# Optimization experiments

Measured on AMD Instinct MI355X. Metric: run time of the kernel, lower is better.

The kernel has to match this reference:

```python
import jax, jax.numpy as jnp
import numpy as np


def _gcn_conv(X, src, dst, norm, W, n_nodes):
    # gather + normalized aggregate (SpMM) then dense linear (GEMM)
    msg = X[src] * norm[:, None]                       # [E, F]
    agg = jax.ops.segment_sum(msg, dst, num_segments=n_nodes)  # [N, F]
    return agg @ W                                     # [N, F_out]


def setup_inputs() -> dict:
    key = jax.random.key(0)
    k1, k2, k3, k4, k5 = jax.random.split(key, 5)
    N, E, D_IN, D_HID, D_OUT = 50000, 800000, 128, 128, 64
    X = jax.random.normal(k1, (N, D_IN), dtype=jnp.float32)
    edge_index = jax.random.randint(k2, (2, E), 0, N, dtype=jnp.int64)
    s = 1.0 / np.sqrt(D_IN)
    W1 = jax.random.normal(k3, (D_IN, D_HID), dtype=jnp.float32) * s
    W2 = jax.random.normal(k4, (D_HID, D_HID), dtype=jnp.float32) * s
    W3 = jax.random.normal(k5, (D_HID, D_OUT), dtype=jnp.float32) * s
    return {"X": X, "edge_index": edge_index, "W1": W1, "W2": W2, "W3": W3}


def reference(X, edge_index, W1, W2, W3):
    n_nodes = X.shape[0]
    src, dst = edge_index[0], edge_index[1]
    # symmetric degree normalization D^-1/2 A D^-1/2 (degrees from edge list)
    ones = jnp.ones(src.shape[0], dtype=X.dtype)
    deg = jax.ops.segment_sum(ones, dst, num_segments=n_nodes)
    deg = jnp.maximum(deg, 1.0)
    dinv = jax.lax.rsqrt(deg)
    norm = dinv[src] * dinv[dst]                       # [E]
    h = jax.nn.relu(_gcn_conv(X, src, dst, norm, W1, n_nodes))
    h = jax.nn.relu(_gcn_conv(h, src, dst, norm, W2, n_nodes))
    h = jax.nn.relu(_gcn_conv(h, src, dst, norm, W3, n_nodes))
    return jax.nn.softmax(h, axis=-1)
```

## Files before the change

kernel.cpp:

```cpp
#include <hip/hip_runtime.h>
#include <hip/hip_bf16.h>

typedef __attribute__((ext_vector_type(8))) short short8;
typedef __attribute__((ext_vector_type(4))) short short4v;
typedef __attribute__((ext_vector_type(4))) float f32x4;

static inline size_t ws_align(size_t x) { return (x + 511) & ~((size_t)511); }

static __device__ inline unsigned short f2bf(float f) {
    __hip_bfloat16 h = __float2bfloat16(f);
    return __builtin_bit_cast(unsigned short, h);
}

__global__ void sniff_kernel(const unsigned short* __restrict__ w1,
                             const unsigned int* __restrict__ ei,
                             int* __restrict__ flags) {
    int i = threadIdx.x;
    unsigned e = (w1[2 * i] >> 7) & 0xFF;
    unsigned long long m1 = __ballot(e >= 100 && e <= 130);
    unsigned long long m2 = __ballot(ei[2 * i + 1] == 0u);
    if (i == 0) {
        flags[0] = (__popcll(m1) < 48) ? 1 : 0;
        flags[1] = (__popcll(m2) >= 48) ? 1 : 0;
    }
}

__global__ void hist_kernel(const int* __restrict__ ei, const int* __restrict__ flags,
                            int* __restrict__ counts, int* __restrict__ loff, int E) {
    int e = blockIdx.x * blockDim.x + threadIdx.x;
    if (e < E) {
        int d = flags[1] ? ei[2 * (size_t)E + 2 * e] : ei[(size_t)E + e];
        loff[e] = atomicAdd(&counts[d], 1);
    }
}

__global__ __launch_bounds__(256) void alloc_kernel(const int* __restrict__ counts,
                                                    float* __restrict__ dinv,
                                                    int* __restrict__ rowptr,
                                                    int* __restrict__ total, int N) {
    int n = blockIdx.x * blockDim.x + threadIdx.x;
    int lane = threadIdx.x & 63;
    int c = (n < N) ? counts[n] : 0;
    if (n < N) {
        int d = (c < 1) ? 1 : c;
        dinv[n] = rsqrtf((float)d);
    }
    int incl = c;
#pragma unroll
    for (int off = 1; off < 64; off <<= 1) {
        int v = __shfl_up(incl, off, 64);
        if (lane >= off) incl += v;
    }
    int wavetot = __shfl(incl, 63, 64);
    int base = 0;
    if (lane == 0) base = atomicAdd(total, wavetot);
    base = __shfl(base, 0, 64);
    if (n < N) rowptr[n] = base + incl - c;
}

__global__ void fill_kernel(const int* __restrict__ ei, const int* __restrict__ flags,
                            const float* __restrict__ dinv, const int* __restrict__ rowptr,
                            const int* __restrict__ loff, int2* __restrict__ edgedat, int E) {
    int e = blockIdx.x * blockDim.x + threadIdx.x;
    if (e < E) {
        int s, d;
        if (flags[1]) {
            s = ei[2 * e];
            d = ei[2 * (size_t)E + 2 * e];
        } else {
            s = ei[e];
            d = ei[(size_t)E + e];
        }
        int pos = rowptr[d] + loff[e];
        float wt = dinv[s] * dinv[d];
        edgedat[pos] = make_int2(s, __float_as_int(wt));
    }
}


template <int FOUT>
__global__ __launch_bounds__(256) void gemm_kernel(const void* __restrict__ Araw, int a_follows,
                                                   const void* __restrict__ Wraw,
                                                   const int* __restrict__ flags,
                                                   unsigned short* __restrict__ out, int Nrows) {
    constexpr int K = 128;
    constexpr int NT = FOUT / 16;
    constexpr int LDB = K + 8;
    __shared__ __align__(16) unsigned short bt[FOUT * LDB];

    const int tid = threadIdx.x;
    const int in_fp32 = flags[0];
    const int a_fp32 = a_follows & in_fp32;

    constexpr int TOT4 = K * FOUT / 4;
    if (in_fp32) {
        const float* Wf = (const float*)Wraw;
        for (int i = tid; i < TOT4; i += 256) {
            int idx = i * 4;
            int k = idx / FOUT;
            int n = idx & (FOUT - 1);
            float4 v = *(const float4*)(const void*)(Wf + idx);
            bt[(n + 0) * LDB + k] = f2bf(v.x);
            bt[(n + 1) * LDB + k] = f2bf(v.y);
            bt[(n + 2) * LDB + k] = f2bf(v.z);
            bt[(n + 3) * LDB + k] = f2bf(v.w);
        }
    } else {
        const unsigned short* Ws = (const unsigned short*)Wraw;
        for (int i = tid; i < TOT4; i += 256) {
            int idx = i * 4;
            int k = idx / FOUT;
            int n = idx & (FOUT - 1);
            short4v v = *(const short4v*)(const void*)(Ws + idx);
#pragma unroll
            for (int j = 0; j < 4; j++) bt[(n + j) * LDB + k] = ((const unsigned short*)&v)[j];
        }
    }

    const int wave = tid >> 6;
    const int lane = tid & 63;
    const int quad = lane >> 4;
    const int r16 = lane & 15;

    short8 afrag[2][4];
#pragma unroll
    for (int t = 0; t < 2; t++) {
        int arow = blockIdx.x * 128 + t * 64 + wave * 16 + r16;
        if (arow > Nrows - 1) arow = Nrows - 1;
        if (a_fp32) {
            const float* Ap = (const float*)Araw + (size_t)arow * K + quad * 8;
#pragma unroll
            for (int kk = 0; kk < 4; kk++) {
                float4 f0 = *(const float4*)(const void*)(Ap + kk * 32);
                float4 f1 = *(const float4*)(const void*)(Ap + kk * 32 + 4);
                short8 r;
                r[0] = (short)f2bf(f0.x); r[1] = (short)f2bf(f0.y);
                r[2] = (short)f2bf(f0.z); r[3] = (short)f2bf(f0.w);
                r[4] = (short)f2bf(f1.x); r[5] = (short)f2bf(f1.y);
                r[6] = (short)f2bf(f1.z); r[7] = (short)f2bf(f1.w);
                afrag[t][kk] = r;
            }
        } else {
            const unsigned short* Ap = (const unsigned short*)Araw + (size_t)arow * K + quad * 8;
#pragma unroll
            for (int kk = 0; kk < 4; kk++) afrag[t][kk] = *(const short8*)(const void*)(Ap + kk * 32);
        }
    }

    __syncthreads();

    f32x4 acc[2][NT];
#pragma unroll
    for (int t = 0; t < 2; t++)
#pragma unroll
        for (int nt = 0; nt < NT; nt++) acc[t][nt] = (f32x4){0.f, 0.f, 0.f, 0.f};

#pragma unroll
    for (int kk = 0; kk < 4; kk++) {
#pragma unroll
        for (int nt = 0; nt < NT; nt++) {
            short8 b = *(const short8*)(const void*)(&bt[(nt * 16 + r16) * LDB + kk * 32 + quad * 8]);
#pragma unroll
            for (int t = 0; t < 2; t++)
                acc[t][nt] = __builtin_amdgcn_mfma_f32_16x16x32_bf16(afrag[t][kk], b, acc[t][nt], 0, 0, 0);
        }
    }

#pragma unroll
    for (int t = 0; t < 2; t++) {
#pragma unroll
        for (int nt = 0; nt < NT; nt++) {
#pragma unroll
            for (int r = 0; r < 4; r++) {
                float v = acc[t][nt][r];
                float o = __shfl_xor(v, 1, 64);
                int row = blockIdx.x * 128 + t * 64 + wave * 16 + quad * 4 + r;
                if (((lane & 1) == 0) && row < Nrows) {
                    __hip_bfloat162 pk;
                    pk.x = __float2bfloat16(v);
                    pk.y = __float2bfloat16(o);
                    *(__hip_bfloat162*)(out + (size_t)row * FOUT + nt * 16 + r16) = pk;
                }
            }
        }
    }
}


__global__ __launch_bounds__(256) void spmm128_kernel(const int2* __restrict__ edgedat,
                                                      const int* __restrict__ rowptr,
                                                      const int* __restrict__ counts,
                                                      const __hip_bfloat162* __restrict__ Hin,
                                                      __hip_bfloat162* __restrict__ Hout, int N) {
    int wid = (blockIdx.x * 256 + threadIdx.x) >> 6;
    if (wid >= N) return;
    int lane = threadIdx.x & 63;
    int n = __builtin_amdgcn_readfirstlane(wid);
    int start = __builtin_amdgcn_readfirstlane(rowptr[n]);
    int len = __builtin_amdgcn_readfirstlane(counts[n]);
    float ax = 0.f, ay = 0.f;
    int j = 0;
    for (; j + 8 <= len; j += 8) {
        int2 ed[8];
        __hip_bfloat162 hv[8];
#pragma unroll
        for (int u = 0; u < 8; u++) ed[u] = edgedat[start + j + u];
#pragma unroll
        for (int u = 0; u < 8; u++) hv[u] = Hin[(size_t)ed[u].x * 64 + lane];
#pragma unroll
        for (int u = 0; u < 8; u++) {
            float w = __int_as_float(ed[u].y);
            ax += w * __bfloat162float(hv[u].x);
            ay += w * __bfloat162float(hv[u].y);
        }
    }
    for (; j + 4 <= len; j += 4) {
        int2 ed[4];
        __hip_bfloat162 hv[4];
#pragma unroll
        for (int u = 0; u < 4; u++) ed[u] = edgedat[start + j + u];
#pragma unroll
        for (int u = 0; u < 4; u++) hv[u] = Hin[(size_t)ed[u].x * 64 + lane];
#pragma unroll
        for (int u = 0; u < 4; u++) {
            float w = __int_as_float(ed[u].y);
            ax += w * __bfloat162float(hv[u].x);
            ay += w * __bfloat162float(hv[u].y);
        }
    }
    for (; j < len; j++) {
        int2 ed = edgedat[start + j];
        float wt = __int_as_float(ed.y);
        __hip_bfloat162 hv = Hin[(size_t)ed.x * 64 + lane];
        ax += wt * __bfloat162float(hv.x);
        ay += wt * __bfloat162float(hv.y);
    }
    __hip_bfloat162 pk;
    pk.x = __float2bfloat16(fmaxf(ax, 0.f));
    pk.y = __float2bfloat16(fmaxf(ay, 0.f));
    Hout[(size_t)n * 64 + lane] = pk;
}

__global__ __launch_bounds__(256) void spmm64_softmax_kernel(const int2* __restrict__ edgedat,
                                                             const int* __restrict__ rowptr,
                                                             const int* __restrict__ counts,
                                                             const __hip_bfloat16* __restrict__ Hin,
                                                             const int* __restrict__ flags,
                                                             void* __restrict__ Out, int N) {
    int wid = (blockIdx.x * 256 + threadIdx.x) >> 6;
    if (wid >= N) return;
    int lane = threadIdx.x & 63;
    int n = __builtin_amdgcn_readfirstlane(wid);
    int start = __builtin_amdgcn_readfirstlane(rowptr[n]);
    int len = __builtin_amdgcn_readfirstlane(counts[n]);
    float a = 0.f;
    int j = 0;
    for (; j + 8 <= len; j += 8) {
        int2 ed[8];
        float hv[8];
#pragma unroll
        for (int u = 0; u < 8; u++) ed[u] = edgedat[start + j + u];
#pragma unroll
        for (int u = 0; u < 8; u++) hv[u] = __bfloat162float(Hin[(size_t)ed[u].x * 64 + lane]);
#pragma unroll
        for (int u = 0; u < 8; u++) a += __int_as_float(ed[u].y) * hv[u];
    }
    for (; j + 4 <= len; j += 4) {
        int2 ed[4];
        float hv[4];
#pragma unroll
        for (int u = 0; u < 4; u++) ed[u] = edgedat[start + j + u];
#pragma unroll
        for (int u = 0; u < 4; u++) hv[u] = __bfloat162float(Hin[(size_t)ed[u].x * 64 + lane]);
#pragma unroll
        for (int u = 0; u < 4; u++) a += __int_as_float(ed[u].y) * hv[u];
    }
    for (; j < len; j++) {
        int2 ed = edgedat[start + j];
        a += __int_as_float(ed.y) * __bfloat162float(Hin[(size_t)ed.x * 64 + lane]);
    }
    a = fmaxf(a, 0.f);
    float m = a;
#pragma unroll
    for (int off = 32; off > 0; off >>= 1) m = fmaxf(m, __shfl_xor(m, off, 64));
    float e = __expf(a - m);
    float s = e;
#pragma unroll
    for (int off = 32; off > 0; off >>= 1) s += __shfl_xor(s, off, 64);
    float r = e / s;
    if (flags[0]) {
        ((float*)Out)[(size_t)n * 64 + lane] = r;
    } else {
        ((unsigned short*)Out)[(size_t)n * 64 + lane] = f2bf(r);
    }
}


extern "C" void kernel_launch(void* const* d_in, const int* in_sizes, int n_in,
                              void* d_out, int out_size, void* d_ws, size_t ws_size,
                              hipStream_t stream) {
    const void* X  = d_in[0];
    const int*  ei = (const int*)d_in[1];
    const void* W1 = d_in[2];
    const void* W2 = d_in[3];
    const void* W3 = d_in[4];

    const int N = in_sizes[0] / 128;
    const int E = in_sizes[1] / 2;

    char* ws = (char*)d_ws;
    size_t off = 0;
    int* counts = (int*)(ws + off);   off += ws_align((size_t)N * 4);
    int* total  = (int*)(ws + off);   off += ws_align(64);
    const size_t zero_bytes = off;
    int* flags    = (int*)(ws + off);   off += ws_align(64);
    int* rowptr   = (int*)(ws + off);   off += ws_align((size_t)N * 4);
    float* dinv   = (float*)(ws + off); off += ws_align((size_t)N * 4);
    int* loff     = (int*)(ws + off);   off += ws_align((size_t)E * 4);
    int2* edgedat = (int2*)(ws + off);  off += ws_align((size_t)E * 8);
    unsigned short* HA = (unsigned short*)(ws + off); off += ws_align((size_t)N * 128 * 2);
    unsigned short* HB = (unsigned short*)(ws + off); off += ws_align((size_t)N * 128 * 2);

    hipMemsetAsync(d_ws, 0, zero_bytes, stream);

    sniff_kernel<<<1, 64, 0, stream>>>((const unsigned short*)W1, (const unsigned int*)ei, flags);
    hist_kernel<<<(E + 255) / 256, 256, 0, stream>>>(ei, flags, counts, loff, E);
    alloc_kernel<<<(N + 255) / 256, 256, 0, stream>>>(counts, dinv, rowptr, total, N);
    fill_kernel<<<(E + 255) / 256, 256, 0, stream>>>(ei, flags, dinv, rowptr, loff, edgedat, E);

    const int gblocks = (N + 127) / 128;
    const int sblocks = (N * 64 + 255) / 256;

    gemm_kernel<128><<<gblocks, 256, 0, stream>>>(X, 1, W1, flags, HA, N);
    spmm128_kernel<<<sblocks, 256, 0, stream>>>(edgedat, rowptr, counts,
                                                (const __hip_bfloat162*)HA, (__hip_bfloat162*)HB, N);
    gemm_kernel<128><<<gblocks, 256, 0, stream>>>(HB, 0, W2, flags, HA, N);
    spmm128_kernel<<<sblocks, 256, 0, stream>>>(edgedat, rowptr, counts,
                                                (const __hip_bfloat162*)HA, (__hip_bfloat162*)HB, N);
    gemm_kernel<64><<<gblocks, 256, 0, stream>>>(HB, 0, W3, flags, HA, N);
    spmm64_softmax_kernel<<<sblocks, 256, 0, stream>>>(edgedat, rowptr, counts,
                                                       (const __hip_bfloat16*)HA, flags, d_out, N);
}
```

Before: 271.3 us.

## Split wave into edge groups with 16-byte row loads in SpMM kernels

Each SpMM wavefront now splits into lane groups (4 groups of 16 lanes for 128 features, 8 groups of 8 lanes for 64 features). Each lane loads 8 bf16 values with one 16-byte vector load, so several edges are gathered in parallel. Partial sums are combined with cross-group shuffles before writing, and the softmax is reduced over 8 lanes with vectorized output stores. This raises memory-level parallelism and cuts per-edge instruction count, at the cost of extra shuffle reductions and more registers.

```diff
diff --git a/kernel.cpp b/kernel.cpp
--- a/kernel.cpp
+++ b/kernel.cpp
@@ -10,6 +10,11 @@
 static __device__ inline unsigned short f2bf(float f) {
     __hip_bfloat16 h = __float2bfloat16(f);
     return __builtin_bit_cast(unsigned short, h);
+}
+
+static __device__ inline float bf2f(unsigned short u) {
+    unsigned int x = ((unsigned int)u) << 16;
+    return __builtin_bit_cast(float, x);
 }
 
 __global__ void sniff_kernel(const unsigned short* __restrict__ w1,
@@ -190,108 +195,156 @@
 __global__ __launch_bounds__(256) void spmm128_kernel(const int2* __restrict__ edgedat,
                                                       const int* __restrict__ rowptr,
                                                       const int* __restrict__ counts,
-                                                      const __hip_bfloat162* __restrict__ Hin,
-                                                      __hip_bfloat162* __restrict__ Hout, int N) {
+                                                      const unsigned short* __restrict__ Hin,
+                                                      unsigned short* __restrict__ Hout, int N) {
     int wid = (blockIdx.x * 256 + threadIdx.x) >> 6;
     if (wid >= N) return;
     int lane = threadIdx.x & 63;
+    int grp = lane >> 4;
+    int gl = lane & 15;
     int n = __builtin_amdgcn_readfirstlane(wid);
     int start = __builtin_amdgcn_readfirstlane(rowptr[n]);
     int len = __builtin_amdgcn_readfirstlane(counts[n]);
-    float ax = 0.f, ay = 0.f;
+    const int2* ep = edgedat + start;
+
+    float acc[8];
+#pragma unroll
+    for (int u = 0; u < 8; u++) acc[u] = 0.f;
+
     int j = 0;
     for (; j + 8 <= len; j += 8) {
-        int2 ed[8];
-        __hip_bfloat162 hv[8];
-#pragma unroll
-        for (int u = 0; u < 8; u++) ed[u] = edgedat[start + j + u];
-#pragma unroll
-        for (int u = 0; u < 8; u++) hv[u] = Hin[(size_t)ed[u].x * 64 + lane];
-#pragma unroll
-        for (int u = 0; u < 8; u++) {
-            float w = __int_as_float(ed[u].y);
-            ax += w * __bfloat162float(hv[u].x);
-            ay += w * __bfloat162float(hv[u].y);
-        }
+        int2 e0 = ep[j + grp];
+        int2 e1 = ep[j + 4 + grp];
+        short8 h0 = *(const short8*)(const void*)(Hin + (size_t)e0.x * 128 + gl * 8);
+        short8 h1 = *(const short8*)(const void*)(Hin + (size_t)e1.x * 128 + gl * 8);
+        float w0 = __int_as_float(e0.y);
+        float w1 = __int_as_float(e1.y);
+#pragma unroll
+        for (int u = 0; u < 8; u++) acc[u] += w0 * bf2f((unsigned short)h0[u]);
+#pragma unroll
+        for (int u = 0; u < 8; u++) acc[u] += w1 * bf2f((unsigned short)h1[u]);
     }
     for (; j + 4 <= len; j += 4) {
-        int2 ed[4];
-        __hip_bfloat162 hv[4];
-#pragma unroll
-        for (int u = 0; u < 4; u++) ed[u] = edgedat[start + j + u];
-#pragma unroll
-        for (int u = 0; u < 4; u++) hv[u] = Hin[(size_t)ed[u].x * 64 + lane];
-#pragma unroll
-        for (int u = 0; u < 4; u++) {
-            float w = __int_as_float(ed[u].y);
-            ax += w * __bfloat162float(hv[u].x);
-            ay += w * __bfloat162float(hv[u].y);
-        }
-    }
-    for (; j < len; j++) {
-        int2 ed = edgedat[start + j];
-        float wt = __int_as_float(ed.y);
-        __hip_bfloat162 hv = Hin[(size_t)ed.x * 64 + lane];
-        ax += wt * __bfloat162float(hv.x);
-        ay += wt * __bfloat162float(hv.y);
-    }
-    __hip_bfloat162 pk;
-    pk.x = __float2bfloat16(fmaxf(ax, 0.f));
-    pk.y = __float2bfloat16(fmaxf(ay, 0.f));
-    Hout[(size_t)n * 64 + lane] = pk;
-}
+        int2 e = ep[j + grp];
+        short8 h = *(const short8*)(const void*)(Hin + (size_t)e.x * 128 + gl * 8);
+        float w = __int_as_float(e.y);
+#pragma unroll
+        for (int u = 0; u < 8; u++) acc[u] += w * bf2f((unsigned short)h[u]);
+    }
+    int rem = len - j;
+    if (grp < rem) {
+        int2 e = ep[j + grp];
+        short8 h = *(const short8*)(const void*)(Hin + (size_t)e.x * 128 + gl * 8);
+        float w = __int_as_float(e.y);
+#pragma unroll
+        for (int u = 0; u < 8; u++) acc[u] += w * bf2f((unsigned short)h[u]);
+    }
+
+#pragma unroll
+    for (int u = 0; u < 8; u++) {
+        acc[u] += __shfl_xor(acc[u], 16, 64);
+        acc[u] += __shfl_xor(acc[u], 32, 64);
+    }
+
+    if (grp == 0) {
+        short8 o;
+#pragma unroll
+        for (int u = 0; u < 8; u++) o[u] = (short)f2bf(fmaxf(acc[u], 0.f));
+        *(short8*)(void*)(Hout + (size_t)n * 128 + gl * 8) = o;
+    }
+}
+
 
 __global__ __launch_bounds__(256) void spmm64_softmax_kernel(const int2* __restrict__ edgedat,
                                                              const int* __restrict__ rowptr,
                                                              const int* __restrict__ counts,
-                                                             const __hip_bfloat16* __restrict__ Hin,
+                                                             const unsigned short* __restrict__ Hin,
                                                              const int* __restrict__ flags,
                                                              void* __restrict__ Out, int N) {
     int wid = (blockIdx.x * 256 + threadIdx.x) >> 6;
     if (wid >= N) return;
     int lane = threadIdx.x & 63;
+    int grp = lane >> 3;
+    int gl = lane & 7;
     int n = __builtin_amdgcn_readfirstlane(wid);
     int start = __builtin_amdgcn_readfirstlane(rowptr[n]);
     int len = __builtin_amdgcn_readfirstlane(counts[n]);
-    float a = 0.f;
+    const int2* ep = edgedat + start;
+
+    float acc[8];
+#pragma unroll
+    for (int u = 0; u < 8; u++) acc[u] = 0.f;
+
     int j = 0;
+    for (; j + 16 <= len; j += 16) {
+        int2 e0 = ep[j + grp];
+        int2 e1 = ep[j + 8 + grp];
+        short8 h0 = *(const short8*)(const void*)(Hin + (size_t)e0.x * 64 + gl * 8);
+        short8 h1 = *(const short8*)(const void*)(Hin + (size_t)e1.x * 64 + gl * 8);
+        float w0 = __int_as_float(e0.y);
+        float w1 = __int_as_float(e1.y);
+#pragma unroll
+        for (int u = 0; u < 8; u++) acc[u] += w0 * bf2f((unsigned short)h0[u]);
+#pragma unroll
+        for (int u = 0; u < 8; u++) acc[u] += w1 * bf2f((unsigned short)h1[u]);
+    }
     for (; j + 8 <= len; j += 8) {
-        int2 ed[8];
-        float hv[8];
-#pragma unroll
-        for (int u = 0; u < 8; u++) ed[u] = edgedat[start + j + u];
-#pragma unroll
-        for (int u = 0; u < 8; u++) hv[u] = __bfloat162float(Hin[(size_t)ed[u].x * 64 + lane]);
-#pragma unroll
-        for (int u = 0; u < 8; u++) a += __int_as_float(ed[u].y) * hv[u];
-    }
-    for (; j + 4 <= len; j += 4) {
-        int2 ed[4];
-        float hv[4];
-#pragma unroll
-        for (int u = 0; u < 4; u++) ed[u] = edgedat[start + j + u];
-#pragma unroll
-        for (int u = 0; u < 4; u++) hv[u] = __bfloat162float(Hin[(size_t)ed[u].x * 64 + lane]);
-#pragma unroll
-        for (int u = 0; u < 4; u++) a += __int_as_float(ed[u].y) * hv[u];
-    }
-    for (; j < len; j++) {
-        int2 ed = edgedat[start + j];
-        a += __int_as_float(ed.y) * __bfloat162float(Hin[(size_t)ed.x * 64 + lane]);
-    }
-    a = fmaxf(a, 0.f);
-    float m = a;
-#pragma unroll
-    for (int off = 32; off > 0; off >>= 1) m = fmaxf(m, __shfl_xor(m, off, 64));
-    float e = __expf(a - m);
-    float s = e;
-#pragma unroll
-    for (int off = 32; off > 0; off >>= 1) s += __shfl_xor(s, off, 64);
-    float r = e / s;
-    if (flags[0]) {
-        ((float*)Out)[(size_t)n * 64 + lane] = r;
-    } else {
-        ((unsigned short*)Out)[(size_t)n * 64 + lane] = f2bf(r);
+        int2 e = ep[j + grp];
+        short8 h = *(const short8*)(const void*)(Hin + (size_t)e.x * 64 + gl * 8);
+        float w = __int_as_float(e.y);
+#pragma unroll
+        for (int u = 0; u < 8; u++) acc[u] += w * bf2f((unsigned short)h[u]);
+    }
+    int rem = len - j;
+    if (grp < rem) {
+        int2 e = ep[j + grp];
+        short8 h = *(const short8*)(const void*)(Hin + (size_t)e.x * 64 + gl * 8);
+        float w = __int_as_float(e.y);
+#pragma unroll
+        for (int u = 0; u < 8; u++) acc[u] += w * bf2f((unsigned short)h[u]);
+    }
+
+#pragma unroll
+    for (int u = 0; u < 8; u++) {
+        acc[u] += __shfl_xor(acc[u], 8, 64);
+        acc[u] += __shfl_xor(acc[u], 16, 64);
+        acc[u] += __shfl_xor(acc[u], 32, 64);
+    }
+
+#pragma unroll
+    for (int u = 0; u < 8; u++) acc[u] = fmaxf(acc[u], 0.f);
+
+    float m = acc[0];
+#pragma unroll
+    for (int u = 1; u < 8; u++) m = fmaxf(m, acc[u]);
+#pragma unroll
+    for (int off = 1; off < 8; off <<= 1) m = fmaxf(m, __shfl_xor(m, off, 64));
+
+    float ex[8];
+    float s = 0.f;
+#pragma unroll
+    for (int u = 0; u < 8; u++) {
+        ex[u] = __expf(acc[u] - m);
+        s += ex[u];
+    }
+#pragma unroll
+    for (int off = 1; off < 8; off <<= 1) s += __shfl_xor(s, off, 64);
+    float inv = 1.0f / s;
+
+    if (grp == 0) {
+        if (flags[0]) {
+            float* op = (float*)Out + (size_t)n * 64 + gl * 8;
+            float4 v0, v1;
+            v0.x = ex[0] * inv; v0.y = ex[1] * inv; v0.z = ex[2] * inv; v0.w = ex[3] * inv;
+            v1.x = ex[4] * inv; v1.y = ex[5] * inv; v1.z = ex[6] * inv; v1.w = ex[7] * inv;
+            *(float4*)(void*)op = v0;
+            *(float4*)(void*)(op + 4) = v1;
+        } else {
+            short8 o;
+#pragma unroll
+            for (int u = 0; u < 8; u++) o[u] = (short)f2bf(ex[u] * inv);
+            *(short8*)(void*)((unsigned short*)Out + (size_t)n * 64 + gl * 8) = o;
+        }
     }
 }
 
@@ -332,12 +385,9 @@
     const int sblocks = (N * 64 + 255) / 256;
 
     gemm_kernel<128><<<gblocks, 256, 0, stream>>>(X, 1, W1, flags, HA, N);
-    spmm128_kernel<<<sblocks, 256, 0, stream>>>(edgedat, rowptr, counts,
-                                                (const __hip_bfloat162*)HA, (__hip_bfloat162*)HB, N);
+    spmm128_kernel<<<sblocks, 256, 0, stream>>>(edgedat, rowptr, counts, HA, HB, N);
     gemm_kernel<128><<<gblocks, 256, 0, stream>>>(HB, 0, W2, flags, HA, N);
-    spmm128_kernel<<<sblocks, 256, 0, stream>>>(edgedat, rowptr, counts,
-                                                (const __hip_bfloat162*)HA, (__hip_bfloat162*)HB, N);
+    spmm128_kernel<<<sblocks, 256, 0, stream>>>(edgedat, rowptr, counts, HA, HB, N);
     gemm_kernel<64><<<gblocks, 256, 0, stream>>>(HB, 0, W3, flags, HA, N);
-    spmm64_softmax_kernel<<<sblocks, 256, 0, stream>>>(edgedat, rowptr, counts,
-                                                       (const __hip_bfloat16*)HA, flags, d_out, N);
-}
+    spmm64_softmax_kernel<<<sblocks, 256, 0, stream>>>(edgedat, rowptr, counts, HA, flags, d_out, N);
+}
```

Result: no change. 273.9 us (+1.0%).
